# Kernel tuning notes

Hardware: AMD Instinct MI355X
Metric: run time of the kernel (lower is better)

## Reference

```python
import jax, jax.numpy as jnp
import numpy as np

# tiny-cuda-nn canonical 2D image hash-grid config
L = 16            # n_levels
F = 2             # n_features_per_level
T = 1 << 19       # hashmap size per level
BASE = 16         # base_resolution
SCALE = 1.5       # per_level_scale
HIDDEN = 64
ENC_DIM = L * F   # 32
OUT = 3           # rgb
S = 1024          # img_res / output_size
PRIME_Y = np.uint32(2654435761)


def setup_inputs() -> dict:
    key = jax.random.key(0)
    k1, k2, k3, k4 = jax.random.split(key, 4)
    # pixel-center grid exactly as in the torch module
    half = 0.5 / S
    xs = jnp.linspace(half, 1.0 - half, S, dtype=jnp.float32)
    xv, yv = jnp.meshgrid(xs, xs, indexing='ij')
    xy = jnp.stack([yv.flatten(), xv.flatten()], axis=1)  # [S*S, 2]
    # tcnn initializes hash tables ~ U(-1e-4, 1e-4)
    hash_tables = jax.random.uniform(k1, (L, T, F), jnp.float32, -1e-4, 1e-4)
    W0 = jax.random.normal(k2, (ENC_DIM, HIDDEN), jnp.float32) * np.sqrt(2.0 / ENC_DIM)
    W1 = jax.random.normal(k3, (HIDDEN, HIDDEN), jnp.float32) * np.sqrt(2.0 / HIDDEN)
    W2 = jax.random.normal(k4, (HIDDEN, OUT), jnp.float32) * np.sqrt(2.0 / HIDDEN)
    return {"xy": xy, "hash_tables": hash_tables, "W0": W0, "W1": W1, "W2": W2}


def _encode(xy, hash_tables):
    # multiresolution hash-grid encoding with bilinear interpolation
    resolutions = jnp.floor(BASE * SCALE ** jnp.arange(L)).astype(jnp.int32)  # [L]
    offs = jnp.array([[0, 0], [0, 1], [1, 0], [1, 1]], jnp.int32)            # [4,2]

    def level(table, res):
        pos = xy * res.astype(xy.dtype)            # [N,2]
        p0 = jnp.floor(pos).astype(jnp.int32)
        w = pos - p0                                # frac weights [N,2]
        corners = p0[:, None, :] + offs[None]       # [N,4,2]
        # hashed index (tcnn spatial hash): x*1 ^ y*PRIME, mod T
        cu = corners.astype(jnp.uint32)
        hidx = ((cu[..., 0] ^ (cu[..., 1] * PRIME_Y)) % np.uint32(T)).astype(jnp.int32)
        # dense index when the grid fits in the table
        didx = corners[..., 0] + corners[..., 1] * (res + 1)
        idx = jnp.where((res + 1) * (res + 1) <= T, didx, hidx)  # [N,4]
        f = table[idx]                               # [N,4,F] gather
        wx, wy = w[:, 0:1], w[:, 1:2]
        wts = jnp.stack([(1 - wx) * (1 - wy), (1 - wx) * wy,
                         wx * (1 - wy), wx * wy], axis=1)  # [N,4,1]
        return jnp.sum(f * wts, axis=1)              # [N,F]

    feats = jax.vmap(level, in_axes=(0, 0), out_axes=1)(hash_tables, resolutions)  # [N,L,F]
    return feats.reshape(feats.shape[0], ENC_DIM)


def reference(xy, hash_tables, W0, W1, W2):
    enc = _encode(xy, hash_tables)                  # [N,32]
    h = jax.nn.relu(enc @ W0)                       # tiny MLP, no bias (FullyFusedMLP)
    h = jax.nn.relu(h @ W1)
    out = h @ W2                                    # [N,3], linear output
    return out.reshape(S, S, OUT).transpose(2, 0, 1)  # [3,S,S]
```

## Files before the change

kernel.cpp:

```cpp
#include <hip/hip_runtime.h>
#include <cstdint>
#include <cstddef>

#define S_DIM 1024
#define NPTS (S_DIM * S_DIM)
#define NLEV 16
#define TBL (1u << 19)
#define TMASK (TBL - 1u)
#define PRIME_Y 2654435761u

typedef float v4f __attribute__((ext_vector_type(4)));
typedef short v8s __attribute__((ext_vector_type(8)));

__device__ __forceinline__ void split2(float a, float b, uint32_t& hi, uint32_t& lo) {
    uint32_t ua = __float_as_uint(a), ub = __float_as_uint(b);
    uint32_t ha = ua & 0xFFFF0000u, hb = ub & 0xFFFF0000u;
    float la = a - __uint_as_float(ha);
    float lb = b - __uint_as_float(hb);
    hi = (ha >> 16) | hb;
    lo = (__float_as_uint(la) >> 16) | (__float_as_uint(lb) & 0xFFFF0000u);
}

__global__ __launch_bounds__(256) void prep_weights(const float* __restrict__ W0,
                                                    const float* __restrict__ W1,
                                                    uint4* __restrict__ ws) {
    const int tid = threadIdx.x;
    const int lane = tid & 63;
    const int m = lane & 15, q = lane >> 4;

    {
        const int tile = tid >> 6;
        const int n = tile * 16 + m;
        uint32_t hi[4], lo[4];
        #pragma unroll
        for (int d = 0; d < 4; ++d) {
            const int k0 = q * 8 + 2 * d;
            split2(W0[k0 * 64 + n], W0[(k0 + 1) * 64 + n], hi[d], lo[d]);
        }
        ws[tid]       = make_uint4(hi[0], hi[1], hi[2], hi[3]);
        ws[256 + tid] = make_uint4(lo[0], lo[1], lo[2], lo[3]);
    }

    #pragma unroll
    for (int rep = 0; rep < 2; ++rep) {
        const int unit = tid + rep * 256;
        const int l2 = unit & 63, frag = unit >> 6;
        const int nt = frag >> 1, ks = frag & 1;
        const int mm = l2 & 15, qq = l2 >> 4;
        const int n = nt * 16 + mm;
        uint32_t hi[4], lo[4];
        #pragma unroll
        for (int d = 0; d < 4; ++d) {
            const int k0 = ks * 32 + qq * 8 + 2 * d;
            split2(W1[k0 * 64 + n], W1[(k0 + 1) * 64 + n], hi[d], lo[d]);
        }
        ws[512 + unit]  = make_uint4(hi[0], hi[1], hi[2], hi[3]);
        ws[1024 + unit] = make_uint4(lo[0], lo[1], lo[2], lo[3]);
    }
}

static __device__ __forceinline__ float2 level_feat(float x, float y, int res,
                                                    const float* __restrict__ tb) {
    const float fr = (float)res;
    const float px = x * fr, py = y * fr;
    const float fx = floorf(px), fy = floorf(py);
    const float wx = px - fx, wy = py - fy;
    const int x0 = (int)fx, y0 = (int)fy;

    int i00, i01, i10, i11;
    const bool dense = ((long long)(res + 1) * (long long)(res + 1) <= (long long)TBL);
    if (dense) {
        const int st = res + 1;
        i00 = x0 + y0 * st;
        i01 = i00 + st;
        i10 = i00 + 1;
        i11 = i01 + 1;
    } else {
        const unsigned a = (unsigned)x0, b = (unsigned)y0;
        const unsigned hb0 = b * PRIME_Y;
        const unsigned hb1 = (b + 1u) * PRIME_Y;
        i00 = (int)((a ^ hb0) & TMASK);
        i01 = (int)((a ^ hb1) & TMASK);
        i10 = (int)(((a + 1u) ^ hb0) & TMASK);
        i11 = (int)(((a + 1u) ^ hb1) & TMASK);
    }

    const float2 f00 = *(const float2*)(tb + 2 * (size_t)i00);
    const float2 f01 = *(const float2*)(tb + 2 * (size_t)i01);
    const float2 f10 = *(const float2*)(tb + 2 * (size_t)i10);
    const float2 f11 = *(const float2*)(tb + 2 * (size_t)i11);

    const float omx = 1.f - wx, omy = 1.f - wy;
    const float w00 = omx * omy, w01 = omx * wy, w10 = wx * omy, w11 = wx * wy;

    float2 e;
    e.x = f00.x * w00 + f01.x * w01 + f10.x * w10 + f11.x * w11;
    e.y = f00.y * w00 + f01.y * w01 + f10.y * w10 + f11.y * w11;
    return e;
}

__global__ __launch_bounds__(256, 3) void ngp_mfma(
    const float* __restrict__ xy,
    const float* __restrict__ tables,
    const float* __restrict__ W2,
    const uint4* __restrict__ ws,
    float* __restrict__ out)
{
    __shared__ alignas(16) uint32_t encLDS[256 * 36];
    __shared__ alignas(16) uint32_t h0LDS[4 * 16 * 36];
    __shared__ alignas(16) float w2t[3 * 64];

    const int tid = threadIdx.x;
    const int lane = tid & 63;
    const int wave = tid >> 6;
    const int m = lane & 15, q = lane >> 4;
    const int blockBase = blockIdx.x * 256;

    if (tid < 192) w2t[(tid % 3) * 64 + (tid / 3)] = W2[tid];

    {
        const int pid = blockBase + tid;
        const float2 p = ((const float2*)xy)[pid];
        constexpr int RES[NLEV] = {16, 24, 36, 54, 81, 121, 182, 273,
                                   410, 615, 922, 1383, 2075, 3113, 4670, 7006};
        uint32_t* row = encLDS + tid * 36;
        #pragma unroll
        for (int g = 0; g < 4; ++g) {
            uint32_t hi[4], lo[4];
            #pragma unroll
            for (int i = 0; i < 4; ++i) {
                const int l = g * 4 + i;
                const float2 e = level_feat(p.x, p.y, RES[l],
                                            tables + (size_t)l * (size_t)(TBL * 2u));
                split2(e.x, e.y, hi[i], lo[i]);
            }
            *((uint4*)(row + 4 * g))      = make_uint4(hi[0], hi[1], hi[2], hi[3]);
            *((uint4*)(row + 16 + 4 * g)) = make_uint4(lo[0], lo[1], lo[2], lo[3]);
        }
    }

    __syncthreads();

    __builtin_amdgcn_sched_barrier(0);

    v8s w0h[4], w0l[4], w1h[8], w1l[8];
    #pragma unroll
    for (int t = 0; t < 4; ++t) {
        w0h[t] = __builtin_bit_cast(v8s, ws[t * 64 + lane]);
        w0l[t] = __builtin_bit_cast(v8s, ws[256 + t * 64 + lane]);
    }
    #pragma unroll
    for (int f = 0; f < 8; ++f) {
        w1h[f] = __builtin_bit_cast(v8s, ws[512 + f * 64 + lane]);
        w1l[f] = __builtin_bit_cast(v8s, ws[1024 + f * 64 + lane]);
    }

    uint32_t* hrow = h0LDS + (wave * 16 + m) * 36;

    #pragma unroll 1
    for (int t = 0; t < 4; ++t) {
        const uint32_t* erow = encLDS + (wave * 64 + t * 16 + m) * 36;
        const v8s eH = __builtin_bit_cast(v8s, *((const uint4*)(erow + q * 4)));
        const v8s eL = __builtin_bit_cast(v8s, *((const uint4*)(erow + 16 + q * 4)));

        v4f acc0[4];
        #pragma unroll
        for (int nt = 0; nt < 4; ++nt) {
            v4f c = {0.f, 0.f, 0.f, 0.f};
            c = __builtin_amdgcn_mfma_f32_16x16x32_bf16(w0l[nt], eH, c, 0, 0, 0);
            c = __builtin_amdgcn_mfma_f32_16x16x32_bf16(w0h[nt], eL, c, 0, 0, 0);
            c = __builtin_amdgcn_mfma_f32_16x16x32_bf16(w0h[nt], eH, c, 0, 0, 0);
            acc0[nt] = c;
        }

        v4f acc1[4];
        #pragma unroll
        for (int nt = 0; nt < 4; ++nt) acc1[nt] = (v4f){0.f, 0.f, 0.f, 0.f};

        #pragma unroll
        for (int ks = 0; ks < 2; ++ks) {
            #pragma unroll
            for (int nh = 0; nh < 2; ++nh) {
                const int nt = ks * 2 + nh;
                const float r0 = fmaxf(acc0[nt][0], 0.f), r1 = fmaxf(acc0[nt][1], 0.f);
                const float r2 = fmaxf(acc0[nt][2], 0.f), r3 = fmaxf(acc0[nt][3], 0.f);
                uint32_t h0w, l0w, h1w, l1w;
                split2(r0, r1, h0w, l0w);
                split2(r2, r3, h1w, l1w);
                *((uint2*)(hrow + nh * 8 + q * 2))      = make_uint2(h0w, h1w);
                *((uint2*)(hrow + 16 + nh * 8 + q * 2)) = make_uint2(l0w, l1w);
            }
            const v8s bH = __builtin_bit_cast(v8s, *((const uint4*)(hrow + q * 4)));
            const v8s bL = __builtin_bit_cast(v8s, *((const uint4*)(hrow + 16 + q * 4)));

            #pragma unroll
            for (int nt = 0; nt < 4; ++nt) {
                v4f c = acc1[nt];
                c = __builtin_amdgcn_mfma_f32_16x16x32_bf16(w1l[nt*2+ks], bH, c, 0, 0, 0);
                c = __builtin_amdgcn_mfma_f32_16x16x32_bf16(w1h[nt*2+ks], bL, c, 0, 0, 0);
                c = __builtin_amdgcn_mfma_f32_16x16x32_bf16(w1h[nt*2+ks], bH, c, 0, 0, 0);
                acc1[nt] = c;
            }
        }

        float o0 = 0.f, o1 = 0.f, o2 = 0.f;
        #pragma unroll
        for (int nt = 0; nt < 4; ++nt) {
            const int n = nt * 16 + q * 4;
            const float4 wa = *((const float4*)(w2t + 0 * 64 + n));
            const float4 wb = *((const float4*)(w2t + 1 * 64 + n));
            const float4 wc = *((const float4*)(w2t + 2 * 64 + n));
            const float h0r = fmaxf(acc1[nt][0], 0.f), h1r = fmaxf(acc1[nt][1], 0.f);
            const float h2r = fmaxf(acc1[nt][2], 0.f), h3r = fmaxf(acc1[nt][3], 0.f);
            o0 = fmaf(h0r, wa.x, fmaf(h1r, wa.y, fmaf(h2r, wa.z, fmaf(h3r, wa.w, o0))));
            o1 = fmaf(h0r, wb.x, fmaf(h1r, wb.y, fmaf(h2r, wb.z, fmaf(h3r, wb.w, o1))));
            o2 = fmaf(h0r, wc.x, fmaf(h1r, wc.y, fmaf(h2r, wc.z, fmaf(h3r, wc.w, o2))));
        }
        o0 += __shfl_xor(o0, 16); o0 += __shfl_xor(o0, 32);
        o1 += __shfl_xor(o1, 16); o1 += __shfl_xor(o1, 32);
        o2 += __shfl_xor(o2, 16); o2 += __shfl_xor(o2, 32);

        if (lane < 16) {
            const int p = blockBase + wave * 64 + t * 16 + lane;
            out[p] = o0;
            out[NPTS + p] = o1;
            out[2 * NPTS + p] = o2;
        }
    }
}

extern "C" void kernel_launch(void* const* d_in, const int* in_sizes, int n_in,
                              void* d_out, int out_size, void* d_ws, size_t ws_size,
                              hipStream_t stream) {
    const float* xy     = (const float*)d_in[0];
    const float* tables = (const float*)d_in[1];
    const float* W0     = (const float*)d_in[2];
    const float* W1     = (const float*)d_in[3];
    const float* W2     = (const float*)d_in[4];
    float* out = (float*)d_out;
    uint4* ws  = (uint4*)d_ws;

    hipLaunchKernelGGL(prep_weights, dim3(1), dim3(256), 0, stream, W0, W1, ws);
    hipLaunchKernelGGL(ngp_mfma, dim3(NPTS / 256), dim3(256), 0, stream,
                       xy, tables, W2, ws, out);
}
```

Measured before the change: 203.4 us.

## Stage W1 fragments in LDS and reuse encoder rows for hidden activations

Layer-1 weight fragments are no longer held in 32 VGPRs per lane. They are copied once per block into a 16KB LDS array and loaded per MFMA, which lowers register pressure so more waves can be resident. The separate h0 scratch buffer is removed: hidden activations are written back into the already-consumed encoder rows. The W2 LDS transpose is replaced by direct float4 loads from global memory, with an opaque zero offset that blocks hoisting. In exchange it adds LDS traffic and global reads of W2 inside the inner loop, and the W1 copy adds global loads at block start.

```diff
diff --git a/kernel.cpp b/kernel.cpp
--- a/kernel.cpp
+++ b/kernel.cpp
@@ -107,8 +107,7 @@
     float* __restrict__ out)
 {
     __shared__ alignas(16) uint32_t encLDS[256 * 36];
-    __shared__ alignas(16) uint32_t h0LDS[4 * 16 * 36];
-    __shared__ alignas(16) float w2t[3 * 64];
+    __shared__ alignas(16) uint4 w1LDS[1024];
 
     const int tid = threadIdx.x;
     const int lane = tid & 63;
@@ -116,7 +115,8 @@
     const int m = lane & 15, q = lane >> 4;
     const int blockBase = blockIdx.x * 256;
 
-    if (tid < 192) w2t[(tid % 3) * 64 + (tid / 3)] = W2[tid];
+    #pragma unroll
+    for (int i = 0; i < 4; ++i) w1LDS[tid + 256 * i] = ws[512 + tid + 256 * i];
 
     {
         const int pid = blockBase + tid;
@@ -143,25 +143,22 @@
 
     __builtin_amdgcn_sched_barrier(0);
 
-    v8s w0h[4], w0l[4], w1h[8], w1l[8];
+    v8s w0h[4], w0l[4];
     #pragma unroll
     for (int t = 0; t < 4; ++t) {
         w0h[t] = __builtin_bit_cast(v8s, ws[t * 64 + lane]);
         w0l[t] = __builtin_bit_cast(v8s, ws[256 + t * 64 + lane]);
     }
-    #pragma unroll
-    for (int f = 0; f < 8; ++f) {
-        w1h[f] = __builtin_bit_cast(v8s, ws[512 + f * 64 + lane]);
-        w1l[f] = __builtin_bit_cast(v8s, ws[1024 + f * 64 + lane]);
-    }
-
-    uint32_t* hrow = h0LDS + (wave * 16 + m) * 36;
 
     #pragma unroll 1
     for (int t = 0; t < 4; ++t) {
-        const uint32_t* erow = encLDS + (wave * 64 + t * 16 + m) * 36;
-        const v8s eH = __builtin_bit_cast(v8s, *((const uint4*)(erow + q * 4)));
-        const v8s eL = __builtin_bit_cast(v8s, *((const uint4*)(erow + 16 + q * 4)));
+        int tOff = 0;
+        asm volatile("" : "+v"(tOff));
+
+        uint32_t* hrow = encLDS + (wave * 64 + t * 16 + m) * 36;
+
+        const v8s eH = __builtin_bit_cast(v8s, *((const uint4*)(hrow + q * 4)));
+        const v8s eL = __builtin_bit_cast(v8s, *((const uint4*)(hrow + 16 + q * 4)));
 
         v4f acc0[4];
         #pragma unroll
@@ -195,10 +192,12 @@
 
             #pragma unroll
             for (int nt = 0; nt < 4; ++nt) {
+                const v8s a_h = __builtin_bit_cast(v8s, w1LDS[tOff + (nt * 2 + ks) * 64 + lane]);
+                const v8s a_l = __builtin_bit_cast(v8s, w1LDS[tOff + 512 + (nt * 2 + ks) * 64 + lane]);
                 v4f c = acc1[nt];
-                c = __builtin_amdgcn_mfma_f32_16x16x32_bf16(w1l[nt*2+ks], bH, c, 0, 0, 0);
-                c = __builtin_amdgcn_mfma_f32_16x16x32_bf16(w1h[nt*2+ks], bL, c, 0, 0, 0);
-                c = __builtin_amdgcn_mfma_f32_16x16x32_bf16(w1h[nt*2+ks], bH, c, 0, 0, 0);
+                c = __builtin_amdgcn_mfma_f32_16x16x32_bf16(a_l, bH, c, 0, 0, 0);
+                c = __builtin_amdgcn_mfma_f32_16x16x32_bf16(a_h, bL, c, 0, 0, 0);
+                c = __builtin_amdgcn_mfma_f32_16x16x32_bf16(a_h, bH, c, 0, 0, 0);
                 acc1[nt] = c;
             }
         }
@@ -206,15 +205,15 @@
         float o0 = 0.f, o1 = 0.f, o2 = 0.f;
         #pragma unroll
         for (int nt = 0; nt < 4; ++nt) {
-            const int n = nt * 16 + q * 4;
-            const float4 wa = *((const float4*)(w2t + 0 * 64 + n));
-            const float4 wb = *((const float4*)(w2t + 1 * 64 + n));
-            const float4 wc = *((const float4*)(w2t + 2 * 64 + n));
+            const int n0 = nt * 16 + q * 4;
+            const float4 g0 = *((const float4*)(W2 + n0 * 3 + tOff));
+            const float4 g1 = *((const float4*)(W2 + n0 * 3 + tOff + 4));
+            const float4 g2 = *((const float4*)(W2 + n0 * 3 + tOff + 8));
             const float h0r = fmaxf(acc1[nt][0], 0.f), h1r = fmaxf(acc1[nt][1], 0.f);
             const float h2r = fmaxf(acc1[nt][2], 0.f), h3r = fmaxf(acc1[nt][3], 0.f);
-            o0 = fmaf(h0r, wa.x, fmaf(h1r, wa.y, fmaf(h2r, wa.z, fmaf(h3r, wa.w, o0))));
-            o1 = fmaf(h0r, wb.x, fmaf(h1r, wb.y, fmaf(h2r, wb.z, fmaf(h3r, wb.w, o1))));
-            o2 = fmaf(h0r, wc.x, fmaf(h1r, wc.y, fmaf(h2r, wc.z, fmaf(h3r, wc.w, o2))));
+            o0 = fmaf(h0r, g0.x, fmaf(h1r, g0.w, fmaf(h2r, g1.z, fmaf(h3r, g2.y, o0))));
+            o1 = fmaf(h0r, g0.y, fmaf(h1r, g1.x, fmaf(h2r, g1.w, fmaf(h3r, g2.z, o1))));
+            o2 = fmaf(h0r, g0.z, fmaf(h1r, g1.y, fmaf(h2r, g2.x, fmaf(h3r, g2.w, o2))));
         }
         o0 += __shfl_xor(o0, 16); o0 += __shfl_xor(o0, 32);
         o1 += __shfl_xor(o1, 16); o1 += __shfl_xor(o1, 32);
```

New measurement: 173.1 us. 14.9% less time.
